# Performance work log

Measured on AMD Instinct MI355X. Metric: run time of the kernel, lower is better.

## Reference

```python
import jax, jax.numpy as jnp
import numpy as np

N, E, D, H = 50000, 800000, 128, 4
DH = D // H
BN_EPS = 1e-5


def setup_inputs() -> dict:
    key = jax.random.key(0)
    ks = jax.random.split(key, 16)
    s = 0.02
    inp = {
        "x": jax.random.normal(ks[0], (N, D), dtype=jnp.float32),
        "edge_index": jax.random.randint(ks[1], (2, E), 0, N, dtype=jnp.int64),
        "Wk": jax.random.normal(ks[2], (D, D), dtype=jnp.float32) * s,
        "bk": jnp.zeros((D,), jnp.float32),
        "Wm": jax.random.normal(ks[3], (D, D), dtype=jnp.float32) * s,
        "bm": jnp.zeros((D,), jnp.float32),
        "Wq": jax.random.normal(ks[4], (D, D), dtype=jnp.float32) * s,
        "bq": jnp.zeros((D,), jnp.float32),
        "W1": jax.random.normal(ks[5], (D, D), dtype=jnp.float32) * s,
        "b1": jnp.zeros((D,), jnp.float32),
        "gamma": jnp.ones((D,), jnp.float32),
        "beta": jnp.zeros((D,), jnp.float32),
        "W2": jax.random.normal(ks[6], (D, D), dtype=jnp.float32) * s,
        "b2": jnp.zeros((D,), jnp.float32),
    }
    return inp


def reference(x, edge_index, Wk, bk, Wm, bm, Wq, bq, W1, b1, gamma, beta, W2, b2):
    src = edge_index[0]  # [E] softmax segment key
    dst = edge_index[1]  # [E] aggregation target
    x_i = x[dst]         # [E, D] (torch code: X[1])
    x_j = x[src]         # [E, D] (torch code: X[0])

    key = (x_i @ Wk + bk).reshape(-1, H, DH)
    msg = (x_j @ Wm + bm).reshape(-1, H, DH)
    query = (x_j @ Wq + bq).reshape(-1, H, DH) / jnp.sqrt(jnp.float32(DH))

    scores = jnp.sum(query * key, axis=2)  # [E, H]

    # segment softmax over src node index (numerically stable)
    smax = jax.ops.segment_max(scores, src, num_segments=N)
    e = jnp.exp(scores - smax[src])
    ssum = jax.ops.segment_sum(e, src, num_segments=N)
    alpha = e / ssum[src]  # [E, H]

    # rescale by per-src-node edge count
    cnt = jax.ops.segment_sum(jnp.ones((scores.shape[0],), jnp.float32), src, num_segments=N)
    alpha = alpha * cnt[src][:, None]

    out_e = (msg * alpha[:, :, None]).reshape(-1, D)  # [E, D]
    out = jax.ops.segment_sum(out_e, dst, num_segments=N)  # [N, D]

    # MLP: Linear -> BatchNorm1d (training-mode batch stats) -> ReLU -> Linear
    h = out @ W1 + b1
    mean = jnp.mean(h, axis=0)
    var = jnp.var(h, axis=0)  # biased variance, as torch BN uses for normalization
    h = (h - mean) * jax.lax.rsqrt(var + BN_EPS) * gamma + beta
    h = jax.nn.relu(h)
    return h @ W2 + b2
```

## Files before the change

kernel.cpp:

```cpp
#include <hip/hip_runtime.h>
#include <hip/hip_bf16.h>

#define N_NODES 50000
#define N_EDGES 800000
#define DIM 128
#define NHEAD 4
#define GEMM_BLOCKS 782
#define HBLOCKS 313
#define EPB 2560
#define NBUCK 196
#define NBUCK2 392
#define NODE_PAD 50432

typedef __bf16 bf16x8 __attribute__((ext_vector_type(8)));
typedef float f32x4 __attribute__((ext_vector_type(4)));

struct WPtrs { const float* w[5]; };

__global__ __launch_bounds__(256) void prep_weights(WPtrs P, __bf16* __restrict__ Wt)
{
  __shared__ __bf16 tileT[16][136];
  const int mat = blockIdx.x >> 3, sl = blockIdx.x & 7;
  const float* W = P.w[mat];
  const int col0 = sl * 16;
  const int t = threadIdx.x;
  #pragma unroll
  for (int i = 0; i < 8; ++i) {
    int id = t + i * 256;
    int k = id >> 4, c = id & 15;
    tileT[c][k] = (__bf16)W[k * 128 + col0 + c];
  }
  __syncthreads();
  int c = t >> 4, kb = t & 15;
  bf16x8 v = *(const bf16x8*)&tileT[c][kb * 8];
  *(bf16x8*)&Wt[(size_t)mat * 16384 + (size_t)(col0 + c) * 128 + kb * 8] = v;
}


__device__ __forceinline__ void stage_Wt_half(const __bf16* __restrict__ Wt,
    int half, __bf16 (*wLDS)[136])
{
  const int t = threadIdx.x;
  const __bf16* base = Wt + (size_t)half * 64 * 128;
  #pragma unroll
  for (int i = 0; i < 4; ++i) {
    int id = t + i * 256;
    int col = id >> 4, kb = id & 15;
    bf16x8 v = ((const bf16x8*)(base + (size_t)col * 128))[kb];
    *(bf16x8*)&wLDS[col][kb * 8] = v;
  }
}

__device__ __forceinline__ void stage_A_f32(const float* __restrict__ A, int row0,
    int nrows, __bf16 (*aLDS)[136])
{
  const int t = threadIdx.x;
  #pragma unroll
  for (int i = 0; i < 4; ++i) {
    int id = t + i * 256;
    int r = id >> 4, cb = id & 15;
    int gr = row0 + r;
    float4 v0 = make_float4(0.f, 0.f, 0.f, 0.f), v1 = v0;
    if (gr < nrows) {
      const float4* row = (const float4*)(A + (size_t)gr * DIM);
      v0 = row[cb * 2];
      v1 = row[cb * 2 + 1];
    }
    bf16x8 o;
    o[0] = (__bf16)v0.x; o[1] = (__bf16)v0.y; o[2] = (__bf16)v0.z; o[3] = (__bf16)v0.w;
    o[4] = (__bf16)v1.x; o[5] = (__bf16)v1.y; o[6] = (__bf16)v1.z; o[7] = (__bf16)v1.w;
    *(bf16x8*)&aLDS[r][cb * 8] = o;
  }
}

__device__ __forceinline__ void stage_A_bf16(const __bf16* __restrict__ A, int row0,
    int nrows, __bf16 (*aLDS)[136])
{
  const int t = threadIdx.x;
  #pragma unroll
  for (int i = 0; i < 4; ++i) {
    int id = t + i * 256;
    int r = id >> 4, cb = id & 15;
    int gr = row0 + r;
    bf16x8 v = {};
    if (gr < nrows) v = ((const bf16x8*)(A + (size_t)gr * DIM))[cb];
    *(bf16x8*)&aLDS[r][cb * 8] = v;
  }
}

__device__ __forceinline__ void mfma_half(const __bf16 (*aLDS)[136],
    const __bf16 (*wLDS)[136], int half, f32x4 acc[8])
{
  const int lane = threadIdx.x & 63, wave = threadIdx.x >> 6;
  const int m = lane & 15, q = lane >> 4;
  #pragma unroll
  for (int kt = 0; kt < 4; ++kt) {
    bf16x8 a = *(const bf16x8*)&aLDS[wave * 16 + m][kt * 32 + q * 8];
    #pragma unroll
    for (int ct = 0; ct < 4; ++ct) {
      bf16x8 b = *(const bf16x8*)&wLDS[ct * 16 + m][kt * 32 + q * 8];
      acc[half * 4 + ct] =
          __builtin_amdgcn_mfma_f32_16x16x32_bf16(a, b, acc[half * 4 + ct], 0, 0, 0);
    }
  }
}

template <typename OutT>
__device__ __forceinline__ void store_tile(f32x4 acc[8],
    const float* __restrict__ bias, float scale, OutT* __restrict__ C,
    int row0, int nrows)
{
  const int lane = threadIdx.x & 63, wave = threadIdx.x >> 6;
  const int m = lane & 15, q = lane >> 4;
  #pragma unroll
  for (int j = 0; j < 8; ++j) {
    int col = (j >> 2) * 64 + (j & 3) * 16 + m;
    float bv = bias[col];
    #pragma unroll
    for (int r = 0; r < 4; ++r) {
      int row = row0 + wave * 16 + q * 4 + r;
      if (row < nrows) C[(size_t)row * DIM + col] = (OutT)((acc[j][r] + bv) * scale);
    }
  }
}

__device__ __forceinline__ void gemm_pass(const __bf16 (*aLDS)[136],
    __bf16 (*wLDS)[136], const __bf16* __restrict__ Wt, f32x4 acc[8])
{
  #pragma unroll
  for (int i = 0; i < 8; ++i) acc[i] = (f32x4){0.f, 0.f, 0.f, 0.f};
  stage_Wt_half(Wt, 0, wLDS);
  __syncthreads();
  mfma_half(aLDS, wLDS, 0, acc);
  __syncthreads();
  stage_Wt_half(Wt, 1, wLDS);
  __syncthreads();
  mfma_half(aLDS, wLDS, 1, acc);
}

__global__ __launch_bounds__(256) void fat1(const int* __restrict__ ei,
    int* __restrict__ hist,
    const __bf16* __restrict__ Wt, const float* __restrict__ x,
    const float* __restrict__ bk, const float* __restrict__ bm,
    const float* __restrict__ bq,
    __bf16* __restrict__ Kn, __bf16* __restrict__ Mn, __bf16* __restrict__ Qn)
{
  __shared__ __bf16 aLDS[64][136];
  __shared__ __bf16 wLDS[64][136];
  const int b = blockIdx.x, t = threadIdx.x;

  if (b < HBLOCKS) {
    int* h = (int*)&aLDS[0][0];
    for (int i = t; i < NBUCK2; i += 256) h[i] = 0;
    __syncthreads();
    #pragma unroll
    for (int i = 0; i < 10; ++i) {
      int e = b * EPB + i * 256 + t;
      if (e < N_EDGES) {
        int s = ei[e], d = ei[N_EDGES + e];
        atomicAdd(&h[s >> 8], 1);
        atomicAdd(&h[NBUCK + (d >> 8)], 1);
      }
    }
    __syncthreads();
    for (int i = t; i < NBUCK2; i += 256) hist[b * NBUCK2 + i] = h[i];
  } else {
    const int gb = b - HBLOCKS;
    const int mat = gb % 3;
    const int row0 = (gb / 3) * 64;
    const float* bias = (mat == 0) ? bk : (mat == 1) ? bm : bq;
    __bf16* out = (mat == 0) ? Kn : (mat == 1) ? Mn : Qn;
    const float scale = (mat == 2) ? 0.17677669529663689f : 1.0f;
    f32x4 acc[8];
    stage_A_f32(x, row0, N_NODES, aLDS);
    gemm_pass(aLDS, wLDS, Wt + (size_t)mat * 16384, acc);
    store_tile<__bf16>(acc, bias, scale, out, row0, N_NODES);
  }
}

__global__ __launch_bounds__(64) void bucket_scan(const int* __restrict__ hist,
    int* __restrict__ bbase, int* __restrict__ tot)
{
  const int b = blockIdx.x, l = threadIdx.x;
  int run = 0;
  for (int c = 0; c < 5; ++c) {
    int idx = c * 64 + l;
    int v = (idx < HBLOCKS) ? hist[idx * NBUCK2 + b] : 0;
    int orig = v;
    #pragma unroll
    for (int o = 1; o < 64; o <<= 1) {
      int n = __shfl_up(v, o);
      if (l >= o) v += n;
    }
    if (idx < HBLOCKS) bbase[idx * NBUCK2 + b] = run + v - orig;
    run += __shfl(v, 63);
  }
  if (l == 0) tot[b] = run;
}

__global__ __launch_bounds__(256) void bucket_starts(const int* __restrict__ tot,
    int* __restrict__ bstart)
{
  __shared__ int s[256];
  const int t = threadIdx.x;
  int v = (t < NBUCK) ? tot[t] : 0;
  s[t] = v; __syncthreads();
  for (int o = 1; o < 256; o <<= 1) {
    int x = (t >= o) ? s[t - o] : 0; __syncthreads();
    s[t] += x; __syncthreads();
  }
  if (t < NBUCK) bstart[t] = s[t] - v;
  __syncthreads();
  v = (t < NBUCK) ? tot[NBUCK + t] : 0;
  s[t] = v; __syncthreads();
  for (int o = 1; o < 256; o <<= 1) {
    int x = (t >= o) ? s[t - o] : 0; __syncthreads();
    s[t] += x; __syncthreads();
  }
  if (t < NBUCK) bstart[NBUCK + t] = s[t] - v;
}

__global__ __launch_bounds__(256) void edge_scatter(const int* __restrict__ ei,
    const int* __restrict__ bbase, const int* __restrict__ bstart,
    int2* __restrict__ bucketedS, int* __restrict__ bucketedD)
{
  __shared__ int base[NBUCK2];
  __shared__ int cur[NBUCK2];
  const int b = blockIdx.x, t = threadIdx.x;
  for (int i = t; i < NBUCK2; i += 256) {
    base[i] = bstart[i] + bbase[b * NBUCK2 + i];
    cur[i] = 0;
  }
  __syncthreads();
  #pragma unroll
  for (int i = 0; i < 10; ++i) {
    int e = b * EPB + i * 256 + t;
    if (e < N_EDGES) {
      int s = ei[e], d = ei[N_EDGES + e];
      int pk = s | (d << 16);
      int bs = s >> 8, bd = NBUCK + (d >> 8);
      int lo = atomicAdd(&cur[bs], 1);
      int ld = atomicAdd(&cur[bd], 1);
      int slotD = base[bd] + ld;
      bucketedS[base[bs] + lo] = make_int2(pk, slotD);
      bucketedD[slotD] = pk;
    }
  }
}

__global__ __launch_bounds__(256) void bucket_rank(const int2* __restrict__ bucketedS,
    const int* __restrict__ bucketedD, const int* __restrict__ bstart,
    const int* __restrict__ tot,
    int2* __restrict__ elistS, int* __restrict__ elistD,
    int* __restrict__ starts, int* __restrict__ deg,
    int* __restrict__ startsD, int* __restrict__ degD)
{
  __shared__ int c1[256], ns[256], c2[256];
  const int b = blockIdx.x, t = threadIdx.x;
  const bool srcSide = (b < NBUCK);
  const int bb = srcSide ? b : b - NBUCK;
  const int seg0 = bstart[b];
  const int cnt = tot[b];

  c1[t] = 0; c2[t] = 0;
  __syncthreads();
  if (srcSide) {
    const int2* ent = bucketedS + seg0;
    for (int i = t; i < cnt; i += 256)
      atomicAdd(&c1[(int)((unsigned)ent[i].x & 0xFFFFu) - (bb << 8)], 1);
  } else {
    const int* ent = bucketedD + seg0;
    for (int i = t; i < cnt; i += 256)
      atomicAdd(&c1[(int)((unsigned)ent[i] >> 16) - (bb << 8)], 1);
  }
  __syncthreads();
  ns[t] = c1[t]; __syncthreads();
  for (int o = 1; o < 256; o <<= 1) {
    int x = (t >= o) ? ns[t - o] : 0; __syncthreads();
    ns[t] += x; __syncthreads();
  }
  {
    int node = (bb << 8) + t;
    int st = seg0 + ns[t] - c1[t];
    if (srcSide) { starts[node] = st; deg[node] = c1[t]; }
    else         { startsD[node] = st; degD[node] = c1[t]; }
  }
  __syncthreads();
  ns[t] -= c1[t];
  __syncthreads();
  if (srcSide) {
    const int2* ent = bucketedS + seg0;
    for (int i = t; i < cnt; i += 256) {
      int2 en = ent[i];
      unsigned pk = (unsigned)en.x;
      int ln = (int)(pk & 0xFFFFu) - (bb << 8);
      int r = atomicAdd(&c2[ln], 1);
      elistS[seg0 + ns[ln] + r] = make_int2((int)(pk >> 16), en.y);
    }
  } else {
    const int* ent = bucketedD + seg0;
    for (int i = t; i < cnt; i += 256) {
      unsigned pk = (unsigned)ent[i];
      int ln = (int)(pk >> 16) - (bb << 8);
      int r = atomicAdd(&c2[ln], 1);
      elistD[seg0 + ns[ln] + r] = (int)(pk & 0xFFFFu) | (i << 16);
    }
  }
}

__global__ __launch_bounds__(256) void src_scores(const int* __restrict__ starts,
    const int* __restrict__ degS, const int2* __restrict__ elistS,
    const __bf16* __restrict__ Qn, const __bf16* __restrict__ Kn,
    float* __restrict__ wexp, float* __restrict__ factor)
{
  const int wave = threadIdx.x >> 6, l = threadIdx.x & 63;
  const int n = blockIdx.x * 4 + wave;
  const int g = l >> 4, il = l & 15;
  const int h = il >> 2;
  const int beg = starts[n], end = beg + degS[n];
  if (beg == end) return;

  bf16x8 q8 = ((const bf16x8*)(Qn + (size_t)n * DIM))[il];
  float wsum = 0.f;

  for (int p0 = beg; p0 < end; p0 += 16) {
    int pp[4]; int2 en[4];
    #pragma unroll
    for (int u = 0; u < 4; ++u) {
      pp[u] = p0 + u * 4 + g;
      en[u] = elistS[min(pp[u], end - 1)];
    }
    bf16x8 kk[4];
    #pragma unroll
    for (int u = 0; u < 4; ++u)
      kk[u] = ((const bf16x8*)(Kn + (size_t)en[u].x * DIM))[il];
    #pragma unroll
    for (int u = 0; u < 4; ++u) {
      float pr = 0.f;
      #pragma unroll
      for (int j = 0; j < 8; ++j) pr += (float)q8[j] * (float)kk[u][j];
      pr += __shfl_xor(pr, 1);
      pr += __shfl_xor(pr, 2);
      float w = (pp[u] < end) ? __expf(pr) : 0.f;
      wsum += w;
      if ((pp[u] < end) && (il & 3) == 0) wexp[(size_t)en[u].y * NHEAD + h] = w;
    }
  }
  wsum += __shfl_xor(wsum, 16);
  wsum += __shfl_xor(wsum, 32);
  if (g == 0 && (il & 3) == 0)
    factor[(size_t)n * NHEAD + h] = (float)(end - beg) / wsum;
}

__global__ __launch_bounds__(256) void agg_gemm_stats(const int* __restrict__ startsD,
    const int* __restrict__ degD, const int* __restrict__ elistD,
    const int* __restrict__ bstart,
    const __bf16* __restrict__ Mn, const float* __restrict__ wexp,
    const float* __restrict__ factor,
    const __bf16* __restrict__ Wt, const float* __restrict__ bias,
    __bf16* __restrict__ C, float* __restrict__ colsum, float* __restrict__ colsq)
{
  __shared__ __bf16 aLDS[64][136];
  __shared__ __bf16 wLDS[64][136];
  __shared__ float csum[128], csq[128];
  const int t = threadIdx.x;
  const int row0 = blockIdx.x * 64;
  const int wave = t >> 6, l = t & 63;
  const int g = l >> 4, il = l & 15;
  const int h = il >> 2;
  const int seg0d = bstart[NBUCK + (row0 >> 8)];

  if (t < 128) { csum[t] = 0.f; csq[t] = 0.f; }

  for (int k = 0; k < 16; ++k) {
    const int n = row0 + wave * 16 + k;
    const int beg = startsD[n], end = beg + degD[n];
    float acc[8];
    #pragma unroll
    for (int j = 0; j < 8; ++j) acc[j] = 0.f;

    for (int q0 = beg; q0 < end; q0 += 16) {
      int qq[4], ss[4]; float ww[4];
      #pragma unroll
      for (int u = 0; u < 4; ++u) {
        qq[u] = q0 + u * 4 + g;
        int cq = min(qq[u], end - 1);
        int v = elistD[cq];
        ss[u] = v & 0xFFFF;
        ww[u] = wexp[(size_t)(seg0d + ((unsigned)v >> 16)) * NHEAD + h];
      }
      float ff[4];
      #pragma unroll
      for (int u = 0; u < 4; ++u) ff[u] = factor[(size_t)ss[u] * NHEAD + h];
      bf16x8 mm[4];
      #pragma unroll
      for (int u = 0; u < 4; ++u)
        mm[u] = ((const bf16x8*)(Mn + (size_t)ss[u] * DIM))[il];
      #pragma unroll
      for (int u = 0; u < 4; ++u) {
        float av = (qq[u] < end) ? ww[u] * ff[u] : 0.f;
        #pragma unroll
        for (int j = 0; j < 8; ++j) acc[j] += (float)mm[u][j] * av;
      }
    }
    #pragma unroll
    for (int j = 0; j < 8; ++j) {
      acc[j] += __shfl_xor(acc[j], 16);
      acc[j] += __shfl_xor(acc[j], 32);
    }
    if (g == 0) {
      bf16x8 o;
      #pragma unroll
      for (int j = 0; j < 8; ++j) o[j] = (__bf16)acc[j];
      *(bf16x8*)&aLDS[wave * 16 + k][il * 8] = o;
    }
  }
  f32x4 acc[8];
  gemm_pass(aLDS, wLDS, Wt, acc);

  const int m = l & 15, q = l >> 4;
  #pragma unroll
  for (int j = 0; j < 8; ++j) {
    int col = (j >> 2) * 64 + (j & 3) * 16 + m;
    float bv = bias[col];
    float s = 0.f, s2 = 0.f;
    #pragma unroll
    for (int r = 0; r < 4; ++r) {
      int row = row0 + wave * 16 + q * 4 + r;
      float hv = acc[j][r] + bv;
      if (row < N_NODES) {
        C[(size_t)row * DIM + col] = (__bf16)hv;
        s += hv; s2 += hv * hv;
      }
    }
    s  += __shfl_xor(s, 16);  s  += __shfl_xor(s, 32);
    s2 += __shfl_xor(s2, 16); s2 += __shfl_xor(s2, 32);
    if (q == 0) {
      atomicAdd(&csum[col], s);
      atomicAdd(&csq[col], s2);
    }
  }
  __syncthreads();
  if (t < 128) {
    atomicAdd(&colsum[t], csum[t]);
    atomicAdd(&colsq[t], csq[t]);
  }
}

__global__ __launch_bounds__(256) void gemm_bn(const __bf16* __restrict__ A,
    const __bf16* __restrict__ Wt, const float* __restrict__ bias,
    float* __restrict__ C, const float* __restrict__ colsum,
    const float* __restrict__ colsq, const float* __restrict__ gamma,
    const float* __restrict__ beta)
{
  __shared__ __bf16 aLDS[64][136];
  __shared__ __bf16 wLDS[64][136];
  __shared__ float sA[128], sB[128];
  const int t = threadIdx.x;
  const int row0 = blockIdx.x * 64;

  if (t < 128) {
    float mean = colsum[t] * (1.0f / N_NODES);
    float var = colsq[t] * (1.0f / N_NODES) - mean * mean;
    float inv = rsqrtf(var + 1e-5f);
    float a = gamma[t] * inv;
    sA[t] = a;
    sB[t] = beta[t] - mean * a;
  }
  __syncthreads();

  {
    const int cb = t & 15;
    float sa[8], sb[8];
    #pragma unroll
    for (int j = 0; j < 8; ++j) { sa[j] = sA[cb * 8 + j]; sb[j] = sB[cb * 8 + j]; }
    #pragma unroll
    for (int i = 0; i < 4; ++i) {
      int id = t + i * 256;
      int r = id >> 4;
      int gr = row0 + r;
      bf16x8 v = {};
      if (gr < N_NODES) v = ((const bf16x8*)(A + (size_t)gr * DIM))[cb];
      bf16x8 o;
      #pragma unroll
      for (int j = 0; j < 8; ++j)
        o[j] = (__bf16)fmaxf((float)v[j] * sa[j] + sb[j], 0.f);
      *(bf16x8*)&aLDS[r][cb * 8] = o;
    }
  }
  f32x4 acc[8];
  gemm_pass(aLDS, wLDS, Wt, acc);
  store_tile<float>(acc, bias, 1.0f, C, row0, N_NODES);
}

extern "C" void kernel_launch(void* const* d_in, const int* in_sizes, int n_in,
                              void* d_out, int out_size, void* d_ws, size_t ws_size,
                              hipStream_t stream) {
  const float* x     = (const float*)d_in[0];
  const int*   ei    = (const int*)d_in[1];
  const float* Wk    = (const float*)d_in[2];
  const float* bk    = (const float*)d_in[3];
  const float* Wm    = (const float*)d_in[4];
  const float* bm    = (const float*)d_in[5];
  const float* Wq    = (const float*)d_in[6];
  const float* bq    = (const float*)d_in[7];
  const float* W1    = (const float*)d_in[8];
  const float* b1    = (const float*)d_in[9];
  const float* gamma = (const float*)d_in[10];
  const float* beta  = (const float*)d_in[11];
  const float* W2    = (const float*)d_in[12];
  const float* b2    = (const float*)d_in[13];

  float* ws = (float*)d_ws;
  const size_t ND  = (size_t)N_NODES * DIM;
  const size_t NDh = ND / 2;
  const size_t EH  = (size_t)N_EDGES * NHEAD;

  __bf16* Kn   = (__bf16*)ws;
  __bf16* Mn   = (__bf16*)(ws + NDh);
  __bf16* Qn   = (__bf16*)(ws + 2 * NDh);
  __bf16* h1   = (__bf16*)(ws + 3 * NDh);
  float*  wexp = ws + 4 * NDh;
  int2*   bucketedS = (int2*)wexp;
  int*    bucketedD = (int*)(bucketedS + N_EDGES);
  int2*   elistS = (int2*)(wexp + EH);
  int*    elistD = (int*)(elistS + N_EDGES);
  int*    hist   = elistD + N_EDGES;
  int*    bbase  = hist + HBLOCKS * NBUCK2;
  int*    tot    = bbase + HBLOCKS * NBUCK2;
  int*    bstart = tot + NBUCK2;
  int*    starts = bstart + NBUCK2;
  int*    deg    = starts + NODE_PAD;
  int*    startsD= deg + NODE_PAD;
  int*    degD   = startsD + NODE_PAD;
  float*  factor = (float*)(degD + NODE_PAD);
  float*  colsum = factor + (size_t)NHEAD * N_NODES;
  float*  colsq  = colsum + 128;
  __bf16* Wt     = (__bf16*)(colsq + 128);
  float*  outp   = (float*)d_out;

  hipMemsetAsync(colsum, 0, 256 * sizeof(float), stream);

  const int node_blocks = N_NODES / 4;

  WPtrs wp; wp.w[0] = Wk; wp.w[1] = Wm; wp.w[2] = Wq; wp.w[3] = W1; wp.w[4] = W2;
  prep_weights<<<40, 256, 0, stream>>>(wp, Wt);

  fat1<<<HBLOCKS + 3 * GEMM_BLOCKS, 256, 0, stream>>>(
      ei, hist, Wt, x, bk, bm, bq, Kn, Mn, Qn);

  bucket_scan<<<NBUCK2, 64, 0, stream>>>(hist, bbase, tot);
  bucket_starts<<<1, 256, 0, stream>>>(tot, bstart);
  edge_scatter<<<HBLOCKS, 256, 0, stream>>>(ei, bbase, bstart, bucketedS, bucketedD);
  bucket_rank<<<NBUCK2, 256, 0, stream>>>(bucketedS, bucketedD, bstart, tot,
                                          elistS, elistD, starts, deg,
                                          startsD, degD);

  src_scores<<<node_blocks, 256, 0, stream>>>(starts, deg, elistS, Qn, Kn,
                                              wexp, factor);

  agg_gemm_stats<<<GEMM_BLOCKS, 256, 0, stream>>>(startsD, degD, elistD, bstart,
                                                  Mn, wexp, factor,
                                                  Wt + 3 * 16384, b1, h1,
                                                  colsum, colsq);
  gemm_bn<<<GEMM_BLOCKS, 256, 0, stream>>>(h1, Wt + 4 * 16384, b2, outp,
                                           colsum, colsq, gamma, beta);
}
```

Before: 291.5 us.

## Aggregate destination rows in LDS per 128-node tile with source-sorted edges

Splits the destination-side ranking into a kernel that groups edges per 128-node destination half-bucket, ordered by source bucket. A new agg_dst kernel accumulates messages into a 128x128 fp32 LDS tile with shared-memory atomics, then writes bf16 aggregates that a separate GEMM+stats kernel consumes. The source ordering is meant to improve locality of the Mn/factor gathers and to avoid per-node serial loops. The cost is many LDS float atomics, an extra global round trip for the aggregate, an extra launch, and only 392 blocks of parallelism.

```diff
diff --git a/kernel.cpp b/kernel.cpp
--- a/kernel.cpp
+++ b/kernel.cpp
@@ -248,31 +248,20 @@
   }
 }
 
-__global__ __launch_bounds__(256) void bucket_rank(const int2* __restrict__ bucketedS,
-    const int* __restrict__ bucketedD, const int* __restrict__ bstart,
-    const int* __restrict__ tot,
-    int2* __restrict__ elistS, int* __restrict__ elistD,
-    int* __restrict__ starts, int* __restrict__ deg,
-    int* __restrict__ startsD, int* __restrict__ degD)
+__global__ __launch_bounds__(256) void bucket_rank_src(const int2* __restrict__ bucketedS,
+    const int* __restrict__ bstart, const int* __restrict__ tot,
+    int2* __restrict__ elistS, int* __restrict__ starts, int* __restrict__ deg)
 {
   __shared__ int c1[256], ns[256], c2[256];
   const int b = blockIdx.x, t = threadIdx.x;
-  const bool srcSide = (b < NBUCK);
-  const int bb = srcSide ? b : b - NBUCK;
   const int seg0 = bstart[b];
   const int cnt = tot[b];
+  const int2* ent = bucketedS + seg0;
 
   c1[t] = 0; c2[t] = 0;
   __syncthreads();
-  if (srcSide) {
-    const int2* ent = bucketedS + seg0;
-    for (int i = t; i < cnt; i += 256)
-      atomicAdd(&c1[(int)((unsigned)ent[i].x & 0xFFFFu) - (bb << 8)], 1);
-  } else {
-    const int* ent = bucketedD + seg0;
-    for (int i = t; i < cnt; i += 256)
-      atomicAdd(&c1[(int)((unsigned)ent[i] >> 16) - (bb << 8)], 1);
-  }
+  for (int i = t; i < cnt; i += 256)
+    atomicAdd(&c1[(int)((unsigned)ent[i].x & 0xFFFFu) - (b << 8)], 1);
   __syncthreads();
   ns[t] = c1[t]; __syncthreads();
   for (int o = 1; o < 256; o <<= 1) {
@@ -280,31 +269,71 @@
     ns[t] += x; __syncthreads();
   }
   {
-    int node = (bb << 8) + t;
-    int st = seg0 + ns[t] - c1[t];
-    if (srcSide) { starts[node] = st; deg[node] = c1[t]; }
-    else         { startsD[node] = st; degD[node] = c1[t]; }
+    int node = (b << 8) + t;
+    starts[node] = seg0 + ns[t] - c1[t];
+    deg[node] = c1[t];
   }
   __syncthreads();
   ns[t] -= c1[t];
   __syncthreads();
-  if (srcSide) {
-    const int2* ent = bucketedS + seg0;
-    for (int i = t; i < cnt; i += 256) {
-      int2 en = ent[i];
-      unsigned pk = (unsigned)en.x;
-      int ln = (int)(pk & 0xFFFFu) - (bb << 8);
-      int r = atomicAdd(&c2[ln], 1);
-      elistS[seg0 + ns[ln] + r] = make_int2((int)(pk >> 16), en.y);
-    }
-  } else {
-    const int* ent = bucketedD + seg0;
-    for (int i = t; i < cnt; i += 256) {
-      unsigned pk = (unsigned)ent[i];
-      int ln = (int)(pk >> 16) - (bb << 8);
-      int r = atomicAdd(&c2[ln], 1);
-      elistD[seg0 + ns[ln] + r] = (int)(pk & 0xFFFFu) | (i << 16);
-    }
+  for (int i = t; i < cnt; i += 256) {
+    int2 en = ent[i];
+    unsigned pk = (unsigned)en.x;
+    int ln = (int)(pk & 0xFFFFu) - (b << 8);
+    int r = atomicAdd(&c2[ln], 1);
+    elistS[seg0 + ns[ln] + r] = make_int2((int)(pk >> 16), en.y);
+  }
+}
+
+__global__ __launch_bounds__(256) void bucket_rank_dstA(const int* __restrict__ bucketedD,
+    const int* __restrict__ bstart, const int* __restrict__ tot,
+    int2* __restrict__ elistA, int* __restrict__ aoff, int* __restrict__ acnt)
+{
+  __shared__ int c1[NBUCK2], c2[NBUCK2];
+  __shared__ int sA[512], sB[512];
+  const int b = blockIdx.x, t = threadIdx.x;
+  const int seg0 = bstart[NBUCK + b];
+  const int cnt = tot[NBUCK + b];
+  const int* ent = bucketedD + seg0;
+
+  for (int i = t; i < NBUCK2; i += 256) { c1[i] = 0; c2[i] = 0; }
+  __syncthreads();
+  for (int i = t; i < cnt; i += 256) {
+    unsigned pk = (unsigned)ent[i];
+    int dl = (int)(pk >> 16) - (b << 8);
+    int sb = (int)(pk & 0xFFFFu) >> 8;
+    atomicAdd(&c1[(dl >> 7) * NBUCK + sb], 1);
+  }
+  __syncthreads();
+  sA[t] = (t < NBUCK2) ? c1[t] : 0;
+  sA[t + 256] = (t + 256 < NBUCK2) ? c1[t + 256] : 0;
+  __syncthreads();
+  int* pin = sA; int* pout = sB;
+  for (int o = 1; o < 512; o <<= 1) {
+    pout[t] = pin[t] + ((t >= o) ? pin[t - o] : 0);
+    int i2 = t + 256;
+    pout[i2] = pin[i2] + ((i2 >= o) ? pin[i2 - o] : 0);
+    __syncthreads();
+    int* tmp = pin; pin = pout; pout = tmp;
+  }
+  int ns0 = pin[t] - c1[t];
+  int ns1 = (t + 256 < NBUCK2) ? (pin[t + 256] - c1[t + 256]) : 0;
+  __syncthreads();
+  c1[t] = ns0;
+  if (t + 256 < NBUCK2) c1[t + 256] = ns1;
+  if (t == 0) {
+    int h0 = pin[NBUCK - 1];
+    aoff[b * 2] = 0;      acnt[b * 2] = h0;
+    aoff[b * 2 + 1] = h0; acnt[b * 2 + 1] = cnt - h0;
+  }
+  __syncthreads();
+  for (int i = t; i < cnt; i += 256) {
+    unsigned pk = (unsigned)ent[i];
+    int src = (int)(pk & 0xFFFFu);
+    int dl = (int)(pk >> 16) - (b << 8);
+    int key = (dl >> 7) * NBUCK + (src >> 8);
+    int r = atomicAdd(&c2[key], 1);
+    elistA[seg0 + c1[key] + r] = make_int2(src | (dl << 16), seg0 + i);
   }
 }
 
@@ -352,11 +381,65 @@
     factor[(size_t)n * NHEAD + h] = (float)(end - beg) / wsum;
 }
 
-__global__ __launch_bounds__(256) void agg_gemm_stats(const int* __restrict__ startsD,
-    const int* __restrict__ degD, const int* __restrict__ elistD,
-    const int* __restrict__ bstart,
+__global__ __launch_bounds__(256) void agg_dst(const int2* __restrict__ elistA,
+    const int* __restrict__ bstart, const int* __restrict__ aoff,
+    const int* __restrict__ acnt,
     const __bf16* __restrict__ Mn, const float* __restrict__ wexp,
-    const float* __restrict__ factor,
+    const float* __restrict__ factor, __bf16* __restrict__ agg)
+{
+  __shared__ float aggL[128][132];
+  const int bb = blockIdx.x, t = threadIdx.x;
+  const int b = bb >> 1, half = bb & 1;
+  const int seg0 = bstart[NBUCK + b];
+  const int e0 = seg0 + aoff[bb], e1 = e0 + acnt[bb];
+
+  for (int i = t; i < 128 * 132; i += 256) ((float*)aggL)[i] = 0.f;
+  __syncthreads();
+
+  const int g16 = t >> 4;
+  const int il = t & 15;
+  const int h = il >> 2;
+
+  for (int p0 = e0; p0 < e1; p0 += 64) {
+    int pp[4]; int2 ea[4];
+    #pragma unroll
+    for (int u = 0; u < 4; ++u) {
+      pp[u] = p0 + u * 16 + g16;
+      ea[u] = elistA[min(pp[u], e1 - 1)];
+    }
+    float ww[4]; bf16x8 mm[4];
+    #pragma unroll
+    for (int u = 0; u < 4; ++u) {
+      int src = ea[u].x & 0xFFFF;
+      ww[u] = wexp[(size_t)ea[u].y * NHEAD + h] * factor[src * NHEAD + h];
+      mm[u] = ((const bf16x8*)(Mn + (size_t)src * DIM))[il];
+    }
+    #pragma unroll
+    for (int u = 0; u < 4; ++u) {
+      if (pp[u] < e1) {
+        int row = ((ea[u].x >> 16) & 0xFF) - half * 128;
+        float* dstp = &aggL[row][il * 8];
+        #pragma unroll
+        for (int j = 0; j < 8; ++j)
+          atomicAdd(&dstp[j], (float)mm[u][j] * ww[u]);
+      }
+    }
+  }
+  __syncthreads();
+
+  for (int i = t; i < 128 * 16; i += 256) {
+    int r = i >> 4, cb = i & 15;
+    int node = (b << 8) + half * 128 + r;
+    if (node < N_NODES) {
+      bf16x8 o;
+      #pragma unroll
+      for (int j = 0; j < 8; ++j) o[j] = (__bf16)aggL[r][cb * 8 + j];
+      *(bf16x8*)(agg + (size_t)node * DIM + cb * 8) = o;
+    }
+  }
+}
+
+__global__ __launch_bounds__(256) void gemm_stats(const __bf16* __restrict__ A,
     const __bf16* __restrict__ Wt, const float* __restrict__ bias,
     __bf16* __restrict__ C, float* __restrict__ colsum, float* __restrict__ colsq)
 {
@@ -365,60 +448,14 @@
   __shared__ float csum[128], csq[128];
   const int t = threadIdx.x;
   const int row0 = blockIdx.x * 64;
-  const int wave = t >> 6, l = t & 63;
-  const int g = l >> 4, il = l & 15;
-  const int h = il >> 2;
-  const int seg0d = bstart[NBUCK + (row0 >> 8)];
-
+
+  stage_A_bf16(A, row0, N_NODES, aLDS);
   if (t < 128) { csum[t] = 0.f; csq[t] = 0.f; }
-
-  for (int k = 0; k < 16; ++k) {
-    const int n = row0 + wave * 16 + k;
-    const int beg = startsD[n], end = beg + degD[n];
-    float acc[8];
-    #pragma unroll
-    for (int j = 0; j < 8; ++j) acc[j] = 0.f;
-
-    for (int q0 = beg; q0 < end; q0 += 16) {
-      int qq[4], ss[4]; float ww[4];
-      #pragma unroll
-      for (int u = 0; u < 4; ++u) {
-        qq[u] = q0 + u * 4 + g;
-        int cq = min(qq[u], end - 1);
-        int v = elistD[cq];
-        ss[u] = v & 0xFFFF;
-        ww[u] = wexp[(size_t)(seg0d + ((unsigned)v >> 16)) * NHEAD + h];
-      }
-      float ff[4];
-      #pragma unroll
-      for (int u = 0; u < 4; ++u) ff[u] = factor[(size_t)ss[u] * NHEAD + h];
-      bf16x8 mm[4];
-      #pragma unroll
-      for (int u = 0; u < 4; ++u)
-        mm[u] = ((const bf16x8*)(Mn + (size_t)ss[u] * DIM))[il];
-      #pragma unroll
-      for (int u = 0; u < 4; ++u) {
-        float av = (qq[u] < end) ? ww[u] * ff[u] : 0.f;
-        #pragma unroll
-        for (int j = 0; j < 8; ++j) acc[j] += (float)mm[u][j] * av;
-      }
-    }
-    #pragma unroll
-    for (int j = 0; j < 8; ++j) {
-      acc[j] += __shfl_xor(acc[j], 16);
-      acc[j] += __shfl_xor(acc[j], 32);
-    }
-    if (g == 0) {
-      bf16x8 o;
-      #pragma unroll
-      for (int j = 0; j < 8; ++j) o[j] = (__bf16)acc[j];
-      *(bf16x8*)&aLDS[wave * 16 + k][il * 8] = o;
-    }
-  }
   f32x4 acc[8];
   gemm_pass(aLDS, wLDS, Wt, acc);
 
-  const int m = l & 15, q = l >> 4;
+  const int lane = t & 63, wave = t >> 6;
+  const int m = lane & 15, q = lane >> 4;
   #pragma unroll
   for (int j = 0; j < 8; ++j) {
     int col = (j >> 2) * 64 + (j & 3) * 16 + m;
@@ -519,21 +556,22 @@
   __bf16* Kn   = (__bf16*)ws;
   __bf16* Mn   = (__bf16*)(ws + NDh);
   __bf16* Qn   = (__bf16*)(ws + 2 * NDh);
-  __bf16* h1   = (__bf16*)(ws + 3 * NDh);
-  float*  wexp = ws + 4 * NDh;
+  __bf16* agg  = (__bf16*)(ws + 3 * NDh);
+  __bf16* h1   = (__bf16*)(ws + 4 * NDh);
+  float*  wexp = ws + 5 * NDh;
   int2*   bucketedS = (int2*)wexp;
   int*    bucketedD = (int*)(bucketedS + N_EDGES);
   int2*   elistS = (int2*)(wexp + EH);
-  int*    elistD = (int*)(elistS + N_EDGES);
-  int*    hist   = elistD + N_EDGES;
+  int2*   elistA = elistS + N_EDGES;
+  int*    hist   = (int*)(elistA + N_EDGES);
   int*    bbase  = hist + HBLOCKS * NBUCK2;
   int*    tot    = bbase + HBLOCKS * NBUCK2;
   int*    bstart = tot + NBUCK2;
-  int*    starts = bstart + NBUCK2;
+  int*    aoff   = bstart + NBUCK2;
+  int*    acnt   = aoff + NBUCK2;
+  int*    starts = acnt + NBUCK2;
   int*    deg    = starts + NODE_PAD;
-  int*    startsD= deg + NODE_PAD;
-  int*    degD   = startsD + NODE_PAD;
-  float*  factor = (float*)(degD + NODE_PAD);
+  float*  factor = (float*)(deg + NODE_PAD);
   float*  colsum = factor + (size_t)NHEAD * N_NODES;
   float*  colsq  = colsum + 128;
   __bf16* Wt     = (__bf16*)(colsq + 128);
@@ -552,17 +590,19 @@
   bucket_scan<<<NBUCK2, 64, 0, stream>>>(hist, bbase, tot);
   bucket_starts<<<1, 256, 0, stream>>>(tot, bstart);
   edge_scatter<<<HBLOCKS, 256, 0, stream>>>(ei, bbase, bstart, bucketedS, bucketedD);
-  bucket_rank<<<NBUCK2, 256, 0, stream>>>(bucketedS, bucketedD, bstart, tot,
-                                          elistS, elistD, starts, deg,
-                                          startsD, degD);
+  bucket_rank_src<<<NBUCK, 256, 0, stream>>>(bucketedS, bstart, tot,
+                                             elistS, starts, deg);
+  bucket_rank_dstA<<<NBUCK, 256, 0, stream>>>(bucketedD, bstart, tot,
+                                              elistA, aoff, acnt);
 
   src_scores<<<node_blocks, 256, 0, stream>>>(starts, deg, elistS, Qn, Kn,
                                               wexp, factor);
 
-  agg_gemm_stats<<<GEMM_BLOCKS, 256, 0, stream>>>(startsD, degD, elistD, bstart,
-                                                  Mn, wexp, factor,
-                                                  Wt + 3 * 16384, b1, h1,
-                                                  colsum, colsq);
+  agg_dst<<<2 * NBUCK, 256, 0, stream>>>(elistA, bstart, aoff, acnt,
+                                         Mn, wexp, factor, agg);
+
+  gemm_stats<<<GEMM_BLOCKS, 256, 0, stream>>>(agg, Wt + 3 * 16384, b1, h1,
+                                              colsum, colsq);
   gemm_bn<<<GEMM_BLOCKS, 256, 0, stream>>>(h1, Wt + 4 * 16384, b2, outp,
                                            colsum, colsq, gamma, beta);
 }
```

Result: slower. 949.4 us (+225.7%).
